# Kernel tuning notes

Measured on AMD Instinct MI355X. Metric: run time of the kernel, lower is better.

Reference implementation:

```python
import jax, jax.numpy as jnp
import numpy as np
from math import factorial

LMAX = 4
N_COEFF = (LMAX + 1) ** 2      # 25 real spherical-harmonic coefficients
N_RADII = 300                  # distance_bins
N_NODES = 512
FEAT = 128
RES_BETA, RES_ALPHA = 180, 360
DIST_STEP = 0.05


def _sh_basis(lmax, y, alpha):
    """Real spherical harmonics evaluated on a (beta, alpha) product grid.
    y = cos(beta) quadrature nodes. Returns [res_beta, res_alpha, (lmax+1)^2]."""
    B, A = len(y), len(alpha)
    P = np.zeros((lmax + 1, lmax + 1, B))
    P[0, 0] = 1.0
    s = np.sqrt(np.clip(1.0 - y * y, 0.0, None))
    for m in range(1, lmax + 1):
        P[m, m] = -(2 * m - 1) * s * P[m - 1, m - 1]
    for m in range(lmax):
        P[m + 1, m] = (2 * m + 1) * y * P[m, m]
    for m in range(lmax + 1):
        for l in range(m + 2, lmax + 1):
            P[l, m] = ((2 * l - 1) * y * P[l - 1, m] - (l + m - 1) * P[l - 2, m]) / (l - m)
    cols = []
    for l in range(lmax + 1):
        for m in range(-l, l + 1):
            am = abs(m)
            Nlm = np.sqrt((2 * l + 1) / (4 * np.pi) * factorial(l - am) / factorial(l + am))
            if m == 0:
                col = Nlm * P[l, 0][:, None] * np.ones((1, A))
            elif m > 0:
                col = np.sqrt(2.0) * Nlm * P[l, m][:, None] * np.cos(m * alpha)[None, :]
            else:
                col = np.sqrt(2.0) * Nlm * P[l, am][:, None] * np.sin(am * alpha)[None, :]
            cols.append(col)
    return np.stack(cols, axis=-1).astype(np.float32)


def setup_inputs() -> dict:
    key = jax.random.key(0)
    ks = jax.random.split(key, 14)

    def lin(k, a, b):
        return jax.random.normal(k, (a, b), jnp.float32) / np.float32(np.sqrt(a))

    x = jax.random.normal(ks[0], (N_NODES, FEAT), jnp.float32)
    fd = [FEAT, 128, 128, 64, 16, 2]
    td = [FEAT, 128, 128, 128, 128, 128, 6]
    fW = [lin(ks[1 + i], fd[i], fd[i + 1]) for i in range(5)]
    tW = [lin(ks[6 + i], td[i], td[i + 1]) for i in range(6)]
    pos_w = lin(ks[12], 2 * FEAT, N_RADII * N_COEFF)
    type_emb = jax.random.normal(ks[13], (5, FEAT), jnp.float32)

    y_np, w_np = np.polynomial.legendre.leggauss(RES_BETA)
    alpha_np = np.linspace(0.0, 2.0 * np.pi, RES_ALPHA, endpoint=False)
    basis = jnp.asarray(_sh_basis(LMAX, y_np, alpha_np))          # [B, A, C]
    qw = jnp.asarray(w_np / 2.0, jnp.float32)                     # gausslegendre / 2
    y_grid = jnp.asarray(y_np, jnp.float32)
    alpha_grid = jnp.asarray(alpha_np, jnp.float32)

    return {
        "x": x,
        "focus_w1": fW[0], "focus_w2": fW[1], "focus_w3": fW[2], "focus_w4": fW[3], "focus_w5": fW[4],
        "type_w1": tW[0], "type_w2": tW[1], "type_w3": tW[2], "type_w4": tW[3], "type_w5": tW[4], "type_w6": tW[5],
        "pos_w": pos_w, "type_emb": type_emb,
        "basis": basis, "qw": qw, "y_grid": y_grid, "alpha_grid": alpha_grid,
        "res_beta": RES_BETA, "res_alpha": RES_ALPHA,
    }


def reference(x, focus_w1, focus_w2, focus_w3, focus_w4, focus_w5,
              type_w1, type_w2, type_w3, type_w4, type_w5, type_w6,
              pos_w, type_emb, basis, qw, y_grid, alpha_grid,
              res_beta, res_alpha):
    n_nodes = x.shape[0]

    # --- focus MLP (relu), per-node logits; STOP logit 0 appended ---
    h = x
    for W in (focus_w1, focus_w2, focus_w3, focus_w4):
        h = jax.nn.relu(h @ W)
    focus_scores = (h @ focus_w5)[:, 0]                             # [n_nodes]
    focus_probs = jax.nn.softmax(jnp.concatenate([focus_scores, jnp.zeros((1,), x.dtype)]))
    focus = jnp.minimum(jnp.argmax(focus_probs), n_nodes - 1)

    # --- type MLP (softplus) on the focus node's features ---
    feat_f = x[focus]                                               # [128]
    th = feat_f
    for W in (type_w1, type_w2, type_w3, type_w4, type_w5):
        th = jax.nn.softplus(th @ W)
    type_dist = jax.nn.softmax(th @ type_w6)                        # [6]
    type_idx = jnp.minimum(jnp.argmax(type_dist), 4)

    # --- position head: SH coefficients per radial shell ---
    pos_in = jnp.concatenate([feat_f, type_emb[type_idx]])          # [256]
    coeffs = (pos_in @ pos_w).reshape(N_RADII, N_COEFF)             # [R, C]

    # to_s2grid: log-density on the sphere for every radial shell
    f = jnp.einsum('rc,bac->rba', coeffs, basis)                    # [R, B, A]
    log_meas = jnp.log(qw)[:, None] + jnp.log(2.0 * jnp.pi / res_alpha)  # [B, 1]

    # radial distribution: integral of exp(f) over the sphere, per shell
    log_radial = jax.nn.logsumexp(f + log_meas[None], axis=(1, 2))  # [R]
    radial_probs = jax.nn.softmax(log_radial)

    key = jax.random.key(42)
    k_r, k_a = jax.random.split(key)
    r_idx = jax.random.categorical(k_r, log_radial)

    # angular distribution at the sampled radius, normalized on S2
    fr = f[r_idx]                                                   # [B, A]
    logZr = jax.nn.logsumexp(fr + log_meas)
    angular_dist = jnp.exp(fr - logZr)                              # [B, A]

    joint_log = (fr + log_meas - logZr).reshape(-1)
    idx = jax.random.categorical(k_a, joint_log)
    y_i = idx // res_alpha
    a_i = idx % res_alpha

    radius_pred = (r_idx.astype(jnp.float32) + 1.0) * DIST_STEP
    return (type_dist, radial_probs, angular_dist, radius_pred, y_grid[y_i], alpha_grid[a_i])
```

## Files before the change

kernel.cpp:

```cpp
#include <hip/hip_runtime.h>
#include <math.h>
#include <stdint.h>

#define NNODES 512
#define FEAT   128
#define NR     300
#define NC     25
#define NB     180
#define NA     360
#define RSPLIT 4
#define BCHUNK (NB / RSPLIT)
#define O_TYPE   0
#define O_RAD    6
#define O_ANG    306
#define O_RADIUS 65106
#define O_Y      65107
#define O_ALPHA  65108

#define WS_KEYS   0
#define WS_FOCUS  4
#define WS_TYPEI  5
#define WS_RIDX   6
#define WS_INVZ   7
#define WS_DEAD   8
#define WS_SCORES 320
#define WS_POSIN  832
#define WS_PV     1280
#define WS_PI     1472
#define WS_Q      1664
#define WS_HR     6176
#define WS_COEF   8352
#define WS_LRP    15872

#define G1_MLP   64
#define G1_PREP  18
#define G1_PFT   21
#define G1_PFP   240
#define G1_TOTAL (G1_MLP + G1_PREP + G1_PFT + G1_PFP)

__constant__ int c_m_of_c[25] = {0,-1,0,1,-2,-1,0,1,2,-3,-2,-1,0,1,2,3,-4,-3,-2,-1,0,1,2,3,4};
__constant__ int c_h_cnt[9] = {5,4,3,2,1,4,3,2,1};
__constant__ int c_h_idx[9][5] = {
  {0,2,6,12,20},
  {3,7,13,21,0},
  {8,14,22,0,0},
  {15,23,0,0,0},
  {24,0,0,0,0},
  {1,5,11,19,0},
  {4,10,18,0,0},
  {9,17,0,0,0},
  {16,0,0,0,0}};

__device__ __forceinline__ void tf2x32(uint32_t k0, uint32_t k1, uint32_t x0, uint32_t x1,
                                       uint32_t& o0, uint32_t& o1) {
  uint32_t ks2 = k0 ^ k1 ^ 0x1BD11BDAu;
#define TF_RND(r) { x0 += x1; x1 = (x1 << r) | (x1 >> (32 - r)); x1 ^= x0; }
  x0 += k0; x1 += k1;
  TF_RND(13) TF_RND(15) TF_RND(26) TF_RND(6)
  x0 += k1; x1 += ks2 + 1u;
  TF_RND(17) TF_RND(29) TF_RND(16) TF_RND(24)
  x0 += ks2; x1 += k0 + 2u;
  TF_RND(13) TF_RND(15) TF_RND(26) TF_RND(6)
  x0 += k0; x1 += k1 + 3u;
  TF_RND(17) TF_RND(29) TF_RND(16) TF_RND(24)
  x0 += k1; x1 += ks2 + 4u;
  TF_RND(13) TF_RND(15) TF_RND(26) TF_RND(6)
  x0 += ks2; x1 += k0 + 5u;
#undef TF_RND
  o0 = x0; o1 = x1;
}

__device__ __forceinline__ float gumbel32(uint32_t k0, uint32_t k1, uint32_t lo) {
  uint32_t o0, o1; tf2x32(k0, k1, 0u, lo, o0, o1);
  uint32_t bits = o0 ^ o1;
  float u = __uint_as_float((bits >> 9) | 0x3f800000u) - 1.0f;
  u = fmaxf(u, 1.1754944e-38f);
  return -logf(-logf(u));
}

__global__ __launch_bounds__(256) void k_front(const float* __restrict__ x,
    const float* __restrict__ w1, const float* __restrict__ w2, const float* __restrict__ w3,
    const float* __restrict__ w4, const float* __restrict__ w5,
    const float* __restrict__ basis, const float* __restrict__ alpha_grid,
    const float* __restrict__ tw1, const float* __restrict__ tw2, const float* __restrict__ tw3,
    const float* __restrict__ tw4, const float* __restrict__ tw5, const float* __restrict__ tw6,
    const float* __restrict__ pos_w,
    float* __restrict__ wsf) {
  __shared__ float A[8][128];
  __shared__ float B[8][128];
  int bx = blockIdx.x, t = threadIdx.x;

  if (bx < G1_MLP) {
    int base = bx * 8;
    for (int i = t; i < 8 * 128; i += 256) A[i >> 7][i & 127] = x[(base + (i >> 7)) * FEAT + (i & 127)];
    __syncthreads();
    int j = t & 127, h = t >> 7;
    {
      float a0 = 0, a1 = 0, a2 = 0, a3 = 0;
#pragma unroll 8
      for (int k = 0; k < 128; k++) {
        float wv = w1[k * 128 + j];
        a0 += A[h * 4 + 0][k] * wv; a1 += A[h * 4 + 1][k] * wv;
        a2 += A[h * 4 + 2][k] * wv; a3 += A[h * 4 + 3][k] * wv;
      }
      __syncthreads();
      B[h * 4 + 0][j] = fmaxf(a0, 0.f); B[h * 4 + 1][j] = fmaxf(a1, 0.f);
      B[h * 4 + 2][j] = fmaxf(a2, 0.f); B[h * 4 + 3][j] = fmaxf(a3, 0.f);
      __syncthreads();
    }
    {
      float a0 = 0, a1 = 0, a2 = 0, a3 = 0;
#pragma unroll 8
      for (int k = 0; k < 128; k++) {
        float wv = w2[k * 128 + j];
        a0 += B[h * 4 + 0][k] * wv; a1 += B[h * 4 + 1][k] * wv;
        a2 += B[h * 4 + 2][k] * wv; a3 += B[h * 4 + 3][k] * wv;
      }
      __syncthreads();
      A[h * 4 + 0][j] = fmaxf(a0, 0.f); A[h * 4 + 1][j] = fmaxf(a1, 0.f);
      A[h * 4 + 2][j] = fmaxf(a2, 0.f); A[h * 4 + 3][j] = fmaxf(a3, 0.f);
      __syncthreads();
    }
    {
      int j3 = t & 63, g = t >> 6;
      float a0 = 0, a1 = 0;
#pragma unroll 8
      for (int k = 0; k < 128; k++) {
        float wv = w3[k * 64 + j3];
        a0 += A[g * 2 + 0][k] * wv; a1 += A[g * 2 + 1][k] * wv;
      }
      __syncthreads();
      B[g * 2 + 0][j3] = fmaxf(a0, 0.f); B[g * 2 + 1][j3] = fmaxf(a1, 0.f);
      __syncthreads();
    }
    {
      int j4 = t & 15, g4 = t >> 4;
      if (g4 < 8) {
        float a0 = 0;
#pragma unroll
        for (int k = 0; k < 64; k++) a0 += B[g4][k] * w4[k * 16 + j4];
        A[g4][j4] = fmaxf(a0, 0.f);
      }
      __syncthreads();
    }
    if (t < 8) {
      float a0 = 0;
#pragma unroll
      for (int k = 0; k < 16; k++) a0 += A[t][k] * w5[k * 2 + 0];
      wsf[WS_SCORES + base + t] = a0;
    }
  } else if (bx < G1_MLP + G1_PREP) {
    int p = (bx - G1_MLP) * 256 + t;
    if (bx == G1_MLP && t == 0) {
      uint32_t* wu = (uint32_t*)wsf;
      uint32_t o0, o1;
      tf2x32(0u, 42u, 0u, 0u, o0, o1); wu[WS_KEYS + 0] = o0; wu[WS_KEYS + 1] = o1;
      tf2x32(0u, 42u, 0u, 1u, o0, o1); wu[WS_KEYS + 2] = o0; wu[WS_KEYS + 3] = o1;
    }
    if (p < NB * NC) {
      int b = p / NC, c = p % NC;
      int m = c_m_of_c[c];
      float q;
      if (m >= 0) {
        q = basis[(b * NA + 0) * NC + c];
      } else {
        float a10 = alpha_grid[10];
        q = basis[(b * NA + 10) * NC + c] / sinf((float)(-m) * a10);
      }
      wsf[WS_Q + p] = q;
    }
  } else if (bx < G1_MLP + G1_PREP + G1_PFT) {
    const float4* mats[5] = {(const float4*)tw1, (const float4*)tw2, (const float4*)tw3,
                             (const float4*)tw4, (const float4*)tw5};
    int lid = (bx - (G1_MLP + G1_PREP)) * 256 + t;
    float acc = 0.f;
    for (int vi = lid; vi < 20672; vi += G1_PFT * 256) {
      int mi = vi >> 12;
      float4 v;
      if (mi < 5) v = mats[mi][vi & 4095];
      else        v = ((const float4*)tw6)[vi - 20480];
      acc += v.x + v.y + v.z + v.w;
    }
    if (acc == -1.2345678e30f) wsf[WS_DEAD] = acc;
  } else {
    int lid = (bx - (G1_MLP + G1_PREP + G1_PFT)) * 256 + t;
    const float4* p4 = (const float4*)pos_w;
    float acc = 0.f;
    for (int i = lid; i < NR * NC * 256 / 4; i += G1_PFP * 256) {
      float4 v = p4[i];
      acc += v.x + v.y + v.z + v.w;
    }
    if (acc == -1.2345678e30f) wsf[WS_DEAD] = acc;
  }
}

__global__ __launch_bounds__(1024) void k_type(const float* __restrict__ x,
    const float* __restrict__ w1, const float* __restrict__ w2, const float* __restrict__ w3,
    const float* __restrict__ w4, const float* __restrict__ w5, const float* __restrict__ w6,
    const float* __restrict__ type_emb, float* __restrict__ out, float* __restrict__ wsf) {
  __shared__ float src[128];
  __shared__ float partial[8][128];
  __shared__ float wrv[16]; __shared__ int wri[16];
  __shared__ float lg[6];
  __shared__ int f_sh, ti_sh;
  int t = threadIdx.x;
  int lane = t & 63, wid = t >> 6;
  float bv = -INFINITY; int bi = 1 << 30;
  if (t < NNODES + 1) { bv = (t < NNODES) ? wsf[WS_SCORES + t] : 0.f; bi = t; }
  for (int off = 32; off; off >>= 1) {
    float v2 = __shfl_down(bv, off); int i2 = __shfl_down(bi, off);
    if (v2 > bv || (v2 == bv && i2 < bi)) { bv = v2; bi = i2; }
  }
  if (lane == 0) { wrv[wid] = bv; wri[wid] = bi; }
  __syncthreads();
  if (t == 0) {
    float v0 = wrv[0]; int i0 = wri[0];
    for (int w = 1; w < 16; w++)
      if (wrv[w] > v0 || (wrv[w] == v0 && wri[w] < i0)) { v0 = wrv[w]; i0 = wri[w]; }
    int focus = (i0 < NNODES - 1) ? i0 : (NNODES - 1);
    ((int*)wsf)[WS_FOCUS] = focus;
    f_sh = focus;
  }
  __syncthreads();
  int focus = f_sh;
  if (t < 128) { float xv = x[focus * FEAT + t]; src[t] = xv; wsf[WS_POSIN + t] = xv; }
  __syncthreads();
  const float* Ws[5] = {w1, w2, w3, w4, w5};
#pragma unroll
  for (int L = 0; L < 5; L++) {
    const float* W = Ws[L];
    int j = t & 127, kc = t >> 7;
    float acc = 0.f;
#pragma unroll
    for (int k = 0; k < 16; k++) acc += src[kc * 16 + k] * W[(kc * 16 + k) * 128 + j];
    partial[kc][j] = acc;
    __syncthreads();
    if (t < 128) {
      float s = 0.f;
#pragma unroll
      for (int q = 0; q < 8; q++) s += partial[q][t];
      src[t] = fmaxf(s, 0.f) + log1pf(expf(-fabsf(s)));
    }
    __syncthreads();
  }
  float prod = 0.f;
  if (t < 768) { int o = t >> 7, j = t & 127; prod = src[j] * w6[j * 6 + o]; }
  for (int off = 32; off; off >>= 1) prod += __shfl_down(prod, off);
  if (t < 768 && lane == 0) wrv[wid] = prod;
  __syncthreads();
  if (t == 0) {
    for (int o = 0; o < 6; o++) lg[o] = wrv[2 * o] + wrv[2 * o + 1];
    float M = lg[0]; int am = 0;
    for (int i = 1; i < 6; i++) if (lg[i] > M) { M = lg[i]; am = i; }
    float e[6], S = 0.f;
    for (int i = 0; i < 6; i++) { e[i] = expf(lg[i] - M); S += e[i]; }
    for (int i = 0; i < 6; i++) out[O_TYPE + i] = e[i] / S;
    int ti = (am < 4) ? am : 4;
    ((int*)wsf)[WS_TYPEI] = ti;
    ti_sh = ti;
  }
  __syncthreads();
  if (t < 128) wsf[WS_POSIN + 128 + t] = type_emb[ti_sh * FEAT + t];
}

__global__ __launch_bounds__(256) void k_coeffs(const float* __restrict__ pos_w,
                                                float* __restrict__ wsf) {
  __shared__ float pin[256];
  __shared__ float partial[4][64];
  int t = threadIdx.x;
  pin[t] = wsf[WS_POSIN + t];
  __syncthreads();
  int oL = t & 63, kc = t >> 6;
  int o = blockIdx.x * 64 + oL;
  float acc = 0.f;
  if (o < NR * NC) {
#pragma unroll 16
    for (int k = 0; k < 64; k++) acc += pin[kc * 64 + k] * pos_w[(kc * 64 + k) * (NR * NC) + o];
  }
  partial[kc][oL] = acc;
  __syncthreads();
  if (kc == 0 && o < NR * NC)
    wsf[WS_COEF + o] = partial[0][oL] + partial[1][oL] + partial[2][oL] + partial[3][oL];
}

__global__ __launch_bounds__(384) void k_radial_lse(const float* __restrict__ qw,
    const float* __restrict__ alpha_grid, float* __restrict__ wsf) {
  __shared__ float4 Hs4[BCHUNK * 3];
  __shared__ float cs[NC];
  __shared__ float wred[6];
  int bx = blockIdx.x;
  int r = bx >> 2, s = bx & 3;
  int b0 = s * BCHUNK;
  int t = threadIdx.x;
  float* Hs = (float*)Hs4;
  if (t < NC) cs[t] = wsf[WS_COEF + r * NC + t];
  __syncthreads();
  const float LOGM = -4.0482054576f;
  for (int p = t; p < BCHUNK * 9; p += 384) {
    int b = p / 9, jj = p % 9;
    int bg = b0 + b;
    int n = c_h_cnt[jj];
    float acc = 0.f;
    for (int q = 0; q < n; q++) { int c = c_h_idx[jj][q]; acc += cs[c] * wsf[WS_Q + bg * NC + c]; }
    if (jj == 0) acc += logf(qw[bg]) + LOGM;
    Hs[b * 12 + jj] = acc;
  }
  __syncthreads();
  float c1 = 0, c2 = 0, c3 = 0, c4 = 0, s1 = 0, s2 = 0, s3 = 0, s4 = 0;
  bool act = t < NA;
  if (act) {
    float al = alpha_grid[t];
    sincosf(al, &s1, &c1);
    sincosf(2.f * al, &s2, &c2);
    sincosf(3.f * al, &s3, &c3);
    sincosf(4.f * al, &s4, &c4);
  }
  float acc = 0.f;
#pragma unroll 5
  for (int b = 0; b < BCHUNK; b++) {
    float4 h0 = Hs4[b * 3 + 0], h1 = Hs4[b * 3 + 1], h2 = Hs4[b * 3 + 2];
    float f = h0.x + h0.y * c1 + h0.z * c2 + h0.w * c3 + h1.x * c4
            + h1.y * s1 + h1.z * s2 + h1.w * s3 + h2.x * s4;
    acc += act ? __expf(f) : 0.f;
  }
  for (int off = 32; off; off >>= 1) acc += __shfl_down(acc, off);
  int wid = t >> 6, lane = t & 63;
  if (lane == 0) wred[wid] = acc;
  __syncthreads();
  if (t == 0) {
    float ss = 0.f;
    for (int w = 0; w < 6; w++) ss += wred[w];
    wsf[WS_LRP + bx] = ss;
  }
}

__global__ __launch_bounds__(384) void k_radial_sample(float* __restrict__ out,
                                                       float* __restrict__ wsf) {
  __shared__ float wred[6]; __shared__ int wri[6];
  __shared__ float fss[NR];
  __shared__ float S_sh; __shared__ int r_sh;
  int t = threadIdx.x, lane = t & 63, wid = t >> 6;
  const uint32_t* wu = (const uint32_t*)wsf;
  uint32_t kr0 = wu[WS_KEYS + 0], kr1 = wu[WS_KEYS + 1];
  float sv = 0.f, lr = -INFINITY;
  if (t < NR) {
    sv = wsf[WS_LRP + 4 * t] + wsf[WS_LRP + 4 * t + 1]
       + wsf[WS_LRP + 4 * t + 2] + wsf[WS_LRP + 4 * t + 3];
    fss[t] = sv;
    lr = logf(sv);
  }
  float ss = sv;
  for (int off = 32; off; off >>= 1) ss += __shfl_down(ss, off);
  if (lane == 0) wred[wid] = ss;
  __syncthreads();
  if (t == 0) {
    float S = 0.f;
    for (int w = 0; w < 6; w++) S += wred[w];
    S_sh = S;
  }
  __syncthreads();
  if (t < NR) out[O_RAD + t] = sv / S_sh;
  float v = (t < NR) ? lr + gumbel32(kr0, kr1, (uint32_t)t) : -INFINITY;
  int bi = (t < NR) ? t : (1 << 30);
  for (int off = 32; off; off >>= 1) {
    float v2 = __shfl_down(v, off); int i2 = __shfl_down(bi, off);
    if (v2 > v || (v2 == v && i2 < bi)) { v = v2; bi = i2; }
  }
  __syncthreads();
  if (lane == 0) { wred[wid] = v; wri[wid] = bi; }
  __syncthreads();
  if (t == 0) {
    float v0 = wred[0]; int i0 = wri[0];
    for (int w = 1; w < 6; w++)
      if (wred[w] > v0 || (wred[w] == v0 && wri[w] < i0)) { v0 = wred[w]; i0 = wri[w]; }
    r_sh = i0;
    ((int*)wsf)[WS_RIDX] = i0;
    out[O_RADIUS] = (float)(i0 + 1) * 0.05f;
    wsf[WS_INVZ] = 1.0f / fss[i0];
  }
  __syncthreads();
  int r = r_sh;
  for (int p = t; p < NB * 9; p += 384) {
    int b = p / 9, jj = p % 9, n = c_h_cnt[jj];
    float acc = 0.f;
    for (int q = 0; q < n; q++) {
      int c = c_h_idx[jj][q];
      acc += wsf[WS_COEF + r * NC + c] * wsf[WS_Q + b * NC + c];
    }
    wsf[WS_HR + b * 12 + jj] = acc;
  }
}

__global__ __launch_bounds__(384) void k_ang_partial(const float* __restrict__ qw,
    const float* __restrict__ alpha_grid, float* __restrict__ out, float* __restrict__ wsf) {
  __shared__ float wrv[6]; __shared__ int wri[6];
  int b = blockIdx.x, t = threadIdx.x;
  int lane = t & 63, wid = t >> 6;
  const uint32_t* wu = (const uint32_t*)wsf;
  uint32_t ka0 = wu[WS_KEYS + 2], ka1 = wu[WS_KEYS + 3];
  const float4* hr4 = (const float4*)(wsf + WS_HR + b * 12);
  float4 h0 = hr4[0], h1 = hr4[1], h2 = hr4[2];
  const float MEAS = 0.01745329252f;
  float elm = qw[b] * MEAS;
  float lm = logf(elm);
  float invZ = wsf[WS_INVZ];
  float v = -INFINITY; int idx = (t < NA) ? b * NA + t : (1 << 30);
  if (t < NA) {
    float al = alpha_grid[t];
    float s1, c1, s2, c2, s3, c3, s4, c4;
    sincosf(al, &s1, &c1); sincosf(2.f * al, &s2, &c2);
    sincosf(3.f * al, &s3, &c3); sincosf(4.f * al, &s4, &c4);
    float f = h0.x + h0.y * c1 + h0.z * c2 + h0.w * c3 + h1.x * c4
            + h1.y * s1 + h1.z * s2 + h1.w * s3 + h2.x * s4;
    out[O_ANG + idx] = __expf(f) * invZ;
    v = f + lm + gumbel32(ka0, ka1, (uint32_t)idx);
  }
  for (int off = 32; off; off >>= 1) {
    float v2 = __shfl_down(v, off); int i2 = __shfl_down(idx, off);
    if (v2 > v || (v2 == v && i2 < idx)) { v = v2; idx = i2; }
  }
  if (lane == 0) { wrv[wid] = v; wri[wid] = idx; }
  __syncthreads();
  if (t == 0) {
    float v0 = wrv[0]; int i0 = wri[0];
    for (int w = 1; w < 6; w++)
      if (wrv[w] > v0 || (wrv[w] == v0 && wri[w] < i0)) { v0 = wrv[w]; i0 = wri[w]; }
    wsf[WS_PV + b] = v0;
    ((int*)wsf)[WS_PI + b] = i0;
  }
}

__global__ __launch_bounds__(256) void k_ang_final(const float* __restrict__ y_grid,
    const float* __restrict__ alpha_grid, float* __restrict__ out, float* __restrict__ wsf) {
  __shared__ float wr[4]; __shared__ int wi[4];
  int t = threadIdx.x, lane = t & 63, wid = t >> 6;
  float v = (t < NB) ? wsf[WS_PV + t] : -INFINITY;
  int i = (t < NB) ? ((const int*)wsf)[WS_PI + t] : (1 << 30);
  for (int off = 32; off; off >>= 1) {
    float v2 = __shfl_down(v, off); int i2 = __shfl_down(i, off);
    if (v2 > v || (v2 == v && i2 < i)) { v = v2; i = i2; }
  }
  if (lane == 0) { wr[wid] = v; wi[wid] = i; }
  __syncthreads();
  if (t == 0) {
    float v0 = wr[0]; int i0 = wi[0];
    for (int w = 1; w < 4; w++)
      if (wr[w] > v0 || (wr[w] == v0 && wi[w] < i0)) { v0 = wr[w]; i0 = wi[w]; }
    int yi = i0 / NA, ai = i0 % NA;
    out[O_Y] = y_grid[yi];
    out[O_ALPHA] = alpha_grid[ai];
  }
}

extern "C" void kernel_launch(void* const* d_in, const int* in_sizes, int n_in,
                              void* d_out, int out_size, void* d_ws, size_t ws_size,
                              hipStream_t stream) {
  const float* x          = (const float*)d_in[0];
  const float* fw1        = (const float*)d_in[1];
  const float* fw2        = (const float*)d_in[2];
  const float* fw3        = (const float*)d_in[3];
  const float* fw4        = (const float*)d_in[4];
  const float* fw5        = (const float*)d_in[5];
  const float* tw1        = (const float*)d_in[6];
  const float* tw2        = (const float*)d_in[7];
  const float* tw3        = (const float*)d_in[8];
  const float* tw4        = (const float*)d_in[9];
  const float* tw5        = (const float*)d_in[10];
  const float* tw6        = (const float*)d_in[11];
  const float* pos_w      = (const float*)d_in[12];
  const float* type_emb   = (const float*)d_in[13];
  const float* basis      = (const float*)d_in[14];
  const float* qw         = (const float*)d_in[15];
  const float* y_grid     = (const float*)d_in[16];
  const float* alpha_grid = (const float*)d_in[17];
  (void)in_sizes; (void)n_in; (void)out_size; (void)ws_size;
  float* out = (float*)d_out;
  float* wsf = (float*)d_ws;

  k_front<<<G1_TOTAL, 256, 0, stream>>>(x, fw1, fw2, fw3, fw4, fw5, basis, alpha_grid,
                                        tw1, tw2, tw3, tw4, tw5, tw6, pos_w, wsf);
  k_type<<<1, 1024, 0, stream>>>(x, tw1, tw2, tw3, tw4, tw5, tw6, type_emb, out, wsf);
  k_coeffs<<<(NR * NC + 63) / 64, 256, 0, stream>>>(pos_w, wsf);
  k_radial_lse<<<NR * RSPLIT, 384, 0, stream>>>(qw, alpha_grid, wsf);
  k_radial_sample<<<1, 384, 0, stream>>>(out, wsf);
  k_ang_partial<<<NB, 384, 0, stream>>>(qw, alpha_grid, out, wsf);
  k_ang_final<<<1, 256, 0, stream>>>(y_grid, alpha_grid, out, wsf);
}
```

Measured before the change: 63.79 us.

## Fuse seven-kernel pipeline into one cooperative kernel with grid syncs

Replaces the chain of seven dependent kernel launches with a single cooperative kernel of 256 blocks, using grid.sync() between the MLP/prep, type head, coefficient GEMV, radial LSE, radial sampling, angular partial and final argmax stages. The aim is to remove per-launch overhead and inter-kernel gaps, which are large relative to this small workload. In exchange, the radial LSE stage now loops over 1200 tasks on 256 blocks, the MLP stage uses smaller per-block tiles, and serial single-block phases leave most of the grid idle at each barrier. The old launch sequence remains as a fallback if the cooperative launch fails.

```diff
diff --git a/kernel.cpp b/kernel.cpp
--- a/kernel.cpp
+++ b/kernel.cpp
@@ -1,6 +1,9 @@
 #include <hip/hip_runtime.h>
+#include <hip/hip_cooperative_groups.h>
 #include <math.h>
 #include <stdint.h>
+
+namespace cg = cooperative_groups;
 
 #define NNODES 512
 #define FEAT   128
@@ -31,6 +34,9 @@
 #define WS_HR     6176
 #define WS_COEF   8352
 #define WS_LRP    15872
+
+#define CG_BLOCKS 256
+#define CG_THREADS 384
 
 #define G1_MLP   64
 #define G1_PREP  18
@@ -78,6 +84,375 @@
   return -logf(-logf(u));
 }
 
+__device__ __forceinline__ float softplusf(float s) {
+  return fmaxf(s, 0.f) + log1pf(expf(-fabsf(s)));
+}
+
+__global__ __launch_bounds__(CG_THREADS) void k_all(
+    const float* __restrict__ x,
+    const float* __restrict__ fw1, const float* __restrict__ fw2, const float* __restrict__ fw3,
+    const float* __restrict__ fw4, const float* __restrict__ fw5,
+    const float* __restrict__ tw1, const float* __restrict__ tw2, const float* __restrict__ tw3,
+    const float* __restrict__ tw4, const float* __restrict__ tw5, const float* __restrict__ tw6,
+    const float* __restrict__ pos_w, const float* __restrict__ type_emb,
+    const float* __restrict__ basis, const float* __restrict__ qw,
+    const float* __restrict__ y_grid, const float* __restrict__ alpha_grid,
+    float* __restrict__ out, float* __restrict__ wsf) {
+  __shared__ float S0[4][128];
+  __shared__ float S1[4][128];
+  __shared__ float4 HS[BCHUNK * 3];
+  __shared__ float cs[32];
+  __shared__ float wred[8]; __shared__ int wri[8];
+  __shared__ float lg[8];
+  __shared__ float fsh[2];
+  __shared__ int ish[2];
+  cg::grid_group grid = cg::this_grid();
+  int bx = blockIdx.x, t = threadIdx.x;
+  int lane = t & 63, wid = t >> 6;
+
+  if (bx < 128) {
+    int base = bx * 4;
+    for (int i = t; i < 512; i += CG_THREADS)
+      S0[i >> 7][i & 127] = x[(base + (i >> 7)) * FEAT + (i & 127)];
+    __syncthreads();
+    int j = t & 127, h = t >> 7;
+    float a0 = 0.f, a1 = 0.f;
+    if (h < 2) {
+#pragma unroll 8
+      for (int k = 0; k < 128; k++) {
+        float wv = fw1[k * 128 + j];
+        a0 += S0[h * 2 + 0][k] * wv; a1 += S0[h * 2 + 1][k] * wv;
+      }
+    }
+    __syncthreads();
+    if (h < 2) { S1[h * 2 + 0][j] = fmaxf(a0, 0.f); S1[h * 2 + 1][j] = fmaxf(a1, 0.f); }
+    __syncthreads();
+    a0 = a1 = 0.f;
+    if (h < 2) {
+#pragma unroll 8
+      for (int k = 0; k < 128; k++) {
+        float wv = fw2[k * 128 + j];
+        a0 += S1[h * 2 + 0][k] * wv; a1 += S1[h * 2 + 1][k] * wv;
+      }
+    }
+    __syncthreads();
+    if (h < 2) { S0[h * 2 + 0][j] = fmaxf(a0, 0.f); S0[h * 2 + 1][j] = fmaxf(a1, 0.f); }
+    __syncthreads();
+    {
+      int j3 = t & 63, g = t >> 6;
+      float a = 0.f;
+      if (g < 4) {
+#pragma unroll 8
+        for (int k = 0; k < 128; k++) a += S0[g][k] * fw3[k * 64 + j3];
+      }
+      __syncthreads();
+      if (g < 4) S1[g][j3] = fmaxf(a, 0.f);
+      __syncthreads();
+    }
+    {
+      int j4 = t & 15, g4 = t >> 4;
+      if (g4 < 4) {
+        float a = 0.f;
+#pragma unroll
+        for (int k = 0; k < 64; k++) a += S1[g4][k] * fw4[k * 16 + j4];
+        S0[g4][j4] = fmaxf(a, 0.f);
+      }
+      __syncthreads();
+    }
+    if (t < 4) {
+      float a = 0.f;
+#pragma unroll
+      for (int k = 0; k < 16; k++) a += S0[t][k] * fw5[k * 2 + 0];
+      wsf[WS_SCORES + base + t] = a;
+    }
+  } else if (bx < 146) {
+    if (bx == 128 && t == 383) {
+      uint32_t* wu = (uint32_t*)wsf;
+      uint32_t o0, o1;
+      tf2x32(0u, 42u, 0u, 0u, o0, o1); wu[WS_KEYS + 0] = o0; wu[WS_KEYS + 1] = o1;
+      tf2x32(0u, 42u, 0u, 1u, o0, o1); wu[WS_KEYS + 2] = o0; wu[WS_KEYS + 3] = o1;
+    }
+    if (t < 256) {
+      int p = (bx - 128) * 256 + t;
+      if (p < NB * NC) {
+        int b = p / NC, c = p % NC;
+        int m = c_m_of_c[c];
+        float q;
+        if (m >= 0) {
+          q = basis[(b * NA + 0) * NC + c];
+        } else {
+          float a10 = alpha_grid[10];
+          q = basis[(b * NA + 10) * NC + c] / sinf((float)(-m) * a10);
+        }
+        wsf[WS_Q + p] = q;
+      }
+    } else {
+      const float4* mats[5] = {(const float4*)tw1, (const float4*)tw2, (const float4*)tw3,
+                               (const float4*)tw4, (const float4*)tw5};
+      int lid = (bx - 128) * 128 + (t - 256);
+      float acc = 0.f;
+      for (int vi = lid; vi < 20672; vi += 18 * 128) {
+        int mi = vi >> 12;
+        float4 v;
+        if (mi < 5) v = mats[mi][vi & 4095];
+        else        v = ((const float4*)tw6)[vi - 20480];
+        acc += v.x + v.y + v.z + v.w;
+      }
+      if (acc == -1.2345678e30f) wsf[WS_DEAD] = acc;
+    }
+  } else {
+    int lid = (bx - 146) * CG_THREADS + t;
+    const float4* p4 = (const float4*)pos_w;
+    float acc = 0.f;
+    for (int i = lid; i < NR * NC * 256 / 4; i += 110 * CG_THREADS) {
+      float4 v = p4[i];
+      acc += v.x + v.y + v.z + v.w;
+    }
+    if (acc == -1.2345678e30f) wsf[WS_DEAD] = acc;
+  }
+  grid.sync();
+
+  if (bx == 0) {
+    float bv = -INFINITY; int bi = 1 << 30;
+    for (int i = t; i < NNODES + 1; i += CG_THREADS) {
+      float v = (i < NNODES) ? wsf[WS_SCORES + i] : 0.f;
+      if (v > bv || (v == bv && i < bi)) { bv = v; bi = i; }
+    }
+    for (int off = 32; off; off >>= 1) {
+      float v2 = __shfl_down(bv, off); int i2 = __shfl_down(bi, off);
+      if (v2 > bv || (v2 == bv && i2 < bi)) { bv = v2; bi = i2; }
+    }
+    if (lane == 0) { wred[wid] = bv; wri[wid] = bi; }
+    __syncthreads();
+    if (t == 0) {
+      float v0 = wred[0]; int i0 = wri[0];
+      for (int w = 1; w < 6; w++)
+        if (wred[w] > v0 || (wred[w] == v0 && wri[w] < i0)) { v0 = wred[w]; i0 = wri[w]; }
+      int focus = (i0 < NNODES - 1) ? i0 : (NNODES - 1);
+      ((int*)wsf)[WS_FOCUS] = focus;
+      ish[0] = focus;
+    }
+    __syncthreads();
+    int focus = ish[0];
+    float* src = &S0[0][0];
+    if (t < 128) { float xv = x[focus * FEAT + t]; src[t] = xv; wsf[WS_POSIN + t] = xv; }
+    __syncthreads();
+    const float* Ws[5] = {tw1, tw2, tw3, tw4, tw5};
+    int kc = t >> 7, j = t & 127;
+#pragma unroll
+    for (int L = 0; L < 5; L++) {
+      const float* W = Ws[L];
+      float acc = 0.f;
+      if (t < 256) {
+#pragma unroll 8
+        for (int k = 0; k < 64; k++) { int kk = kc * 64 + k; acc += src[kk] * W[kk * 128 + j]; }
+        S1[kc][j] = acc;
+      }
+      __syncthreads();
+      if (t < 128) src[t] = softplusf(S1[0][t] + S1[1][t]);
+      __syncthreads();
+    }
+    {
+      int o = t >> 6, l = t & 63;
+      float pr = src[l] * tw6[l * 6 + o] + src[l + 64] * tw6[(l + 64) * 6 + o];
+      for (int off = 32; off; off >>= 1) pr += __shfl_down(pr, off);
+      if (lane == 0) lg[o] = pr;
+    }
+    __syncthreads();
+    if (t == 0) {
+      float M = lg[0]; int am = 0;
+      for (int i = 1; i < 6; i++) if (lg[i] > M) { M = lg[i]; am = i; }
+      float e[6], S = 0.f;
+      for (int i = 0; i < 6; i++) { e[i] = expf(lg[i] - M); S += e[i]; }
+      for (int i = 0; i < 6; i++) out[O_TYPE + i] = e[i] / S;
+      int ti = (am < 4) ? am : 4;
+      ((int*)wsf)[WS_TYPEI] = ti;
+      ish[1] = ti;
+    }
+    __syncthreads();
+    if (t < 128) wsf[WS_POSIN + 128 + t] = type_emb[ish[1] * FEAT + t];
+  }
+  grid.sync();
+
+  if (bx < 118) {
+    float* pin = &S0[0][0];
+    float* part = &S1[0][0];
+    if (t < 256) pin[t] = wsf[WS_POSIN + t];
+    __syncthreads();
+    int oL = t & 63, kc = (t >> 6) & 3;
+    int o = bx * 64 + oL;
+    if (t < 256) {
+      float acc = 0.f;
+      if (o < NR * NC) {
+#pragma unroll 16
+        for (int k = 0; k < 64; k++) { int kk = kc * 64 + k; acc += pin[kk] * pos_w[kk * (NR * NC) + o]; }
+      }
+      part[kc * 64 + oL] = acc;
+    }
+    __syncthreads();
+    if (t < 64 && o < NR * NC)
+      wsf[WS_COEF + o] = part[oL] + part[64 + oL] + part[128 + oL] + part[192 + oL];
+  }
+  grid.sync();
+
+  {
+    float c1 = 0, c2 = 0, c3 = 0, c4 = 0, s1 = 0, s2 = 0, s3 = 0, s4 = 0;
+    bool act = t < NA;
+    if (act) {
+      float al = alpha_grid[t];
+      sincosf(al, &s1, &c1);
+      sincosf(2.f * al, &s2, &c2);
+      sincosf(3.f * al, &s3, &c3);
+      sincosf(4.f * al, &s4, &c4);
+    }
+    const float LOGM = -4.0482054576f;
+    float* Hs = (float*)HS;
+    for (int task = bx; task < NR * RSPLIT; task += CG_BLOCKS) {
+      int r = task >> 2, sb = task & 3, b0 = sb * BCHUNK;
+      __syncthreads();
+      if (t < NC) cs[t] = wsf[WS_COEF + r * NC + t];
+      __syncthreads();
+      for (int p = t; p < BCHUNK * 9; p += CG_THREADS) {
+        int b = p / 9, jj = p % 9;
+        int bg = b0 + b;
+        int n = c_h_cnt[jj];
+        float acc = 0.f;
+        for (int q = 0; q < n; q++) { int c = c_h_idx[jj][q]; acc += cs[c] * wsf[WS_Q + bg * NC + c]; }
+        if (jj == 0) acc += logf(qw[bg]) + LOGM;
+        Hs[b * 12 + jj] = acc;
+      }
+      __syncthreads();
+      float acc = 0.f;
+#pragma unroll 5
+      for (int b = 0; b < BCHUNK; b++) {
+        float4 h0 = HS[b * 3 + 0], h1 = HS[b * 3 + 1], h2 = HS[b * 3 + 2];
+        float f = h0.x + h0.y * c1 + h0.z * c2 + h0.w * c3 + h1.x * c4
+                + h1.y * s1 + h1.z * s2 + h1.w * s3 + h2.x * s4;
+        acc += act ? __expf(f) : 0.f;
+      }
+      for (int off = 32; off; off >>= 1) acc += __shfl_down(acc, off);
+      if (lane == 0) wred[wid] = acc;
+      __syncthreads();
+      if (t == 0) {
+        float ss = 0.f;
+        for (int w = 0; w < 6; w++) ss += wred[w];
+        wsf[WS_LRP + task] = ss;
+      }
+    }
+  }
+  grid.sync();
+
+  if (bx == 0) {
+    const uint32_t* wu = (const uint32_t*)wsf;
+    uint32_t kr0 = wu[WS_KEYS + 0], kr1 = wu[WS_KEYS + 1];
+    float* fss = &S0[0][0];
+    float sv = 0.f, lr = -INFINITY;
+    if (t < NR) {
+      sv = wsf[WS_LRP + 4 * t] + wsf[WS_LRP + 4 * t + 1]
+         + wsf[WS_LRP + 4 * t + 2] + wsf[WS_LRP + 4 * t + 3];
+      fss[t] = sv;
+      lr = logf(sv);
+    }
+    float ss = sv;
+    for (int off = 32; off; off >>= 1) ss += __shfl_down(ss, off);
+    if (lane == 0) wred[wid] = ss;
+    __syncthreads();
+    if (t == 0) {
+      float S = 0.f;
+      for (int w = 0; w < 6; w++) S += wred[w];
+      fsh[0] = S;
+    }
+    __syncthreads();
+    if (t < NR) out[O_RAD + t] = sv / fsh[0];
+    float v = (t < NR) ? lr + gumbel32(kr0, kr1, (uint32_t)t) : -INFINITY;
+    int bi = (t < NR) ? t : (1 << 30);
+    for (int off = 32; off; off >>= 1) {
+      float v2 = __shfl_down(v, off); int i2 = __shfl_down(bi, off);
+      if (v2 > v || (v2 == v && i2 < bi)) { v = v2; bi = i2; }
+    }
+    __syncthreads();
+    if (lane == 0) { wred[wid] = v; wri[wid] = bi; }
+    __syncthreads();
+    if (t == 0) {
+      float v0 = wred[0]; int i0 = wri[0];
+      for (int w = 1; w < 6; w++)
+        if (wred[w] > v0 || (wred[w] == v0 && wri[w] < i0)) { v0 = wred[w]; i0 = wri[w]; }
+      ish[0] = i0;
+      ((int*)wsf)[WS_RIDX] = i0;
+      out[O_RADIUS] = (float)(i0 + 1) * 0.05f;
+      wsf[WS_INVZ] = 1.0f / fss[i0];
+    }
+    __syncthreads();
+    int r = ish[0];
+    for (int p = t; p < NB * 9; p += CG_THREADS) {
+      int b = p / 9, jj = p % 9, n = c_h_cnt[jj];
+      float acc = 0.f;
+      for (int q = 0; q < n; q++) {
+        int c = c_h_idx[jj][q];
+        acc += wsf[WS_COEF + r * NC + c] * wsf[WS_Q + b * NC + c];
+      }
+      wsf[WS_HR + b * 12 + jj] = acc;
+    }
+  }
+  grid.sync();
+
+  if (bx < NB) {
+    int b = bx;
+    const uint32_t* wu = (const uint32_t*)wsf;
+    uint32_t ka0 = wu[WS_KEYS + 2], ka1 = wu[WS_KEYS + 3];
+    const float4* hr4 = (const float4*)(wsf + WS_HR + b * 12);
+    float4 h0 = hr4[0], h1 = hr4[1], h2 = hr4[2];
+    const float MEAS = 0.01745329252f;
+    float elm = qw[b] * MEAS;
+    float lm = logf(elm);
+    float invZ = wsf[WS_INVZ];
+    float v = -INFINITY; int idx = (t < NA) ? b * NA + t : (1 << 30);
+    if (t < NA) {
+      float al = alpha_grid[t];
+      float s1, c1, s2, c2, s3, c3, s4, c4;
+      sincosf(al, &s1, &c1); sincosf(2.f * al, &s2, &c2);
+      sincosf(3.f * al, &s3, &c3); sincosf(4.f * al, &s4, &c4);
+      float f = h0.x + h0.y * c1 + h0.z * c2 + h0.w * c3 + h1.x * c4
+              + h1.y * s1 + h1.z * s2 + h1.w * s3 + h2.x * s4;
+      out[O_ANG + idx] = __expf(f) * invZ;
+      v = f + lm + gumbel32(ka0, ka1, (uint32_t)idx);
+    }
+    for (int off = 32; off; off >>= 1) {
+      float v2 = __shfl_down(v, off); int i2 = __shfl_down(idx, off);
+      if (v2 > v || (v2 == v && i2 < idx)) { v = v2; idx = i2; }
+    }
+    if (lane == 0) { wred[wid] = v; wri[wid] = idx; }
+    __syncthreads();
+    if (t == 0) {
+      float v0 = wred[0]; int i0 = wri[0];
+      for (int w = 1; w < 6; w++)
+        if (wred[w] > v0 || (wred[w] == v0 && wri[w] < i0)) { v0 = wred[w]; i0 = wri[w]; }
+      wsf[WS_PV + b] = v0;
+      ((int*)wsf)[WS_PI + b] = i0;
+    }
+  }
+  grid.sync();
+
+  if (bx == 0) {
+    float v = (t < NB) ? wsf[WS_PV + t] : -INFINITY;
+    int i = (t < NB) ? ((const int*)wsf)[WS_PI + t] : (1 << 30);
+    for (int off = 32; off; off >>= 1) {
+      float v2 = __shfl_down(v, off); int i2 = __shfl_down(i, off);
+      if (v2 > v || (v2 == v && i2 < i)) { v = v2; i = i2; }
+    }
+    if (lane == 0) { wred[wid] = v; wri[wid] = i; }
+    __syncthreads();
+    if (t == 0) {
+      float v0 = wred[0]; int i0 = wri[0];
+      for (int w = 1; w < 6; w++)
+        if (wred[w] > v0 || (wred[w] == v0 && wri[w] < i0)) { v0 = wred[w]; i0 = wri[w]; }
+      int yi = i0 / NA, ai = i0 % NA;
+      out[O_Y] = y_grid[yi];
+      out[O_ALPHA] = alpha_grid[ai];
+    }
+  }
+}
+
 __global__ __launch_bounds__(256) void k_front(const float* __restrict__ x,
     const float* __restrict__ w1, const float* __restrict__ w2, const float* __restrict__ w3,
     const float* __restrict__ w4, const float* __restrict__ w5,
@@ -89,7 +464,6 @@
   __shared__ float A[8][128];
   __shared__ float B[8][128];
   int bx = blockIdx.x, t = threadIdx.x;
-
   if (bx < G1_MLP) {
     int base = bx * 8;
     for (int i = t; i < 8 * 128; i += 256) A[i >> 7][i & 127] = x[(base + (i >> 7)) * FEAT + (i & 127)];
@@ -147,7 +521,7 @@
       float a0 = 0;
 #pragma unroll
       for (int k = 0; k < 16; k++) a0 += A[t][k] * w5[k * 2 + 0];
-      wsf[WS_SCORES + base + t] = a0;
+      wsf[WS_SCORES + bx * 8 + t] = a0;
     }
   } else if (bx < G1_MLP + G1_PREP) {
     int p = (bx - G1_MLP) * 256 + t;
@@ -161,9 +535,8 @@
       int b = p / NC, c = p % NC;
       int m = c_m_of_c[c];
       float q;
-      if (m >= 0) {
-        q = basis[(b * NA + 0) * NC + c];
-      } else {
+      if (m >= 0) q = basis[(b * NA + 0) * NC + c];
+      else {
         float a10 = alpha_grid[10];
         q = basis[(b * NA + 10) * NC + c] / sinf((float)(-m) * a10);
       }
@@ -200,7 +573,7 @@
     const float* __restrict__ type_emb, float* __restrict__ out, float* __restrict__ wsf) {
   __shared__ float src[128];
   __shared__ float partial[8][128];
-  __shared__ float wrv[16]; __shared__ int wri[16];
+  __shared__ float wrv[16]; __shared__ int wri2[16];
   __shared__ float lg[6];
   __shared__ int f_sh, ti_sh;
   int t = threadIdx.x;
@@ -211,12 +584,12 @@
     float v2 = __shfl_down(bv, off); int i2 = __shfl_down(bi, off);
     if (v2 > bv || (v2 == bv && i2 < bi)) { bv = v2; bi = i2; }
   }
-  if (lane == 0) { wrv[wid] = bv; wri[wid] = bi; }
+  if (lane == 0) { wrv[wid] = bv; wri2[wid] = bi; }
   __syncthreads();
   if (t == 0) {
-    float v0 = wrv[0]; int i0 = wri[0];
+    float v0 = wrv[0]; int i0 = wri2[0];
     for (int w = 1; w < 16; w++)
-      if (wrv[w] > v0 || (wrv[w] == v0 && wri[w] < i0)) { v0 = wrv[w]; i0 = wri[w]; }
+      if (wrv[w] > v0 || (wrv[w] == v0 && wri2[w] < i0)) { v0 = wrv[w]; i0 = wri2[w]; }
     int focus = (i0 < NNODES - 1) ? i0 : (NNODES - 1);
     ((int*)wsf)[WS_FOCUS] = focus;
     f_sh = focus;
@@ -239,7 +612,7 @@
       float s = 0.f;
 #pragma unroll
       for (int q = 0; q < 8; q++) s += partial[q][t];
-      src[t] = fmaxf(s, 0.f) + log1pf(expf(-fabsf(s)));
+      src[t] = softplusf(s);
     }
     __syncthreads();
   }
@@ -336,7 +709,7 @@
 
 __global__ __launch_bounds__(384) void k_radial_sample(float* __restrict__ out,
                                                        float* __restrict__ wsf) {
-  __shared__ float wred[6]; __shared__ int wri[6];
+  __shared__ float wred[6]; __shared__ int wri2[6];
   __shared__ float fss[NR];
   __shared__ float S_sh; __shared__ int r_sh;
   int t = threadIdx.x, lane = t & 63, wid = t >> 6;
@@ -367,12 +740,12 @@
     if (v2 > v || (v2 == v && i2 < bi)) { v = v2; bi = i2; }
   }
   __syncthreads();
-  if (lane == 0) { wred[wid] = v; wri[wid] = bi; }
+  if (lane == 0) { wred[wid] = v; wri2[wid] = bi; }
   __syncthreads();
   if (t == 0) {
-    float v0 = wred[0]; int i0 = wri[0];
+    float v0 = wred[0]; int i0 = wri2[0];
     for (int w = 1; w < 6; w++)
-      if (wred[w] > v0 || (wred[w] == v0 && wri[w] < i0)) { v0 = wred[w]; i0 = wri[w]; }
+      if (wred[w] > v0 || (wred[w] == v0 && wri2[w] < i0)) { v0 = wred[w]; i0 = wri2[w]; }
     r_sh = i0;
     ((int*)wsf)[WS_RIDX] = i0;
     out[O_RADIUS] = (float)(i0 + 1) * 0.05f;
@@ -393,7 +766,7 @@
 
 __global__ __launch_bounds__(384) void k_ang_partial(const float* __restrict__ qw,
     const float* __restrict__ alpha_grid, float* __restrict__ out, float* __restrict__ wsf) {
-  __shared__ float wrv[6]; __shared__ int wri[6];
+  __shared__ float wrv[6]; __shared__ int wri2[6];
   int b = blockIdx.x, t = threadIdx.x;
   int lane = t & 63, wid = t >> 6;
   const uint32_t* wu = (const uint32_t*)wsf;
@@ -419,12 +792,12 @@
     float v2 = __shfl_down(v, off); int i2 = __shfl_down(idx, off);
     if (v2 > v || (v2 == v && i2 < idx)) { v = v2; idx = i2; }
   }
-  if (lane == 0) { wrv[wid] = v; wri[wid] = idx; }
+  if (lane == 0) { wrv[wid] = v; wri2[wid] = idx; }
   __syncthreads();
   if (t == 0) {
-    float v0 = wrv[0]; int i0 = wri[0];
+    float v0 = wrv[0]; int i0 = wri2[0];
     for (int w = 1; w < 6; w++)
-      if (wrv[w] > v0 || (wrv[w] == v0 && wri[w] < i0)) { v0 = wrv[w]; i0 = wri[w]; }
+      if (wrv[w] > v0 || (wrv[w] == v0 && wri2[w] < i0)) { v0 = wrv[w]; i0 = wri2[w]; }
     wsf[WS_PV + b] = v0;
     ((int*)wsf)[WS_PI + b] = i0;
   }
@@ -477,12 +850,20 @@
   float* out = (float*)d_out;
   float* wsf = (float*)d_ws;
 
-  k_front<<<G1_TOTAL, 256, 0, stream>>>(x, fw1, fw2, fw3, fw4, fw5, basis, alpha_grid,
-                                        tw1, tw2, tw3, tw4, tw5, tw6, pos_w, wsf);
-  k_type<<<1, 1024, 0, stream>>>(x, tw1, tw2, tw3, tw4, tw5, tw6, type_emb, out, wsf);
-  k_coeffs<<<(NR * NC + 63) / 64, 256, 0, stream>>>(pos_w, wsf);
-  k_radial_lse<<<NR * RSPLIT, 384, 0, stream>>>(qw, alpha_grid, wsf);
-  k_radial_sample<<<1, 384, 0, stream>>>(out, wsf);
-  k_ang_partial<<<NB, 384, 0, stream>>>(qw, alpha_grid, out, wsf);
-  k_ang_final<<<1, 256, 0, stream>>>(y_grid, alpha_grid, out, wsf);
-}
+  void* kargs[] = {(void*)&x, (void*)&fw1, (void*)&fw2, (void*)&fw3, (void*)&fw4, (void*)&fw5,
+                   (void*)&tw1, (void*)&tw2, (void*)&tw3, (void*)&tw4, (void*)&tw5, (void*)&tw6,
+                   (void*)&pos_w, (void*)&type_emb, (void*)&basis, (void*)&qw,
+                   (void*)&y_grid, (void*)&alpha_grid, (void*)&out, (void*)&wsf};
+  hipError_t err = hipLaunchCooperativeKernel((const void*)k_all, dim3(CG_BLOCKS), dim3(CG_THREADS),
+                                              kargs, 0, stream);
+  if (err != hipSuccess) {
+    k_front<<<G1_TOTAL, 256, 0, stream>>>(x, fw1, fw2, fw3, fw4, fw5, basis, alpha_grid,
+                                          tw1, tw2, tw3, tw4, tw5, tw6, pos_w, wsf);
+    k_type<<<1, 1024, 0, stream>>>(x, tw1, tw2, tw3, tw4, tw5, tw6, type_emb, out, wsf);
+    k_coeffs<<<(NR * NC + 63) / 64, 256, 0, stream>>>(pos_w, wsf);
+    k_radial_lse<<<NR * RSPLIT, 384, 0, stream>>>(qw, alpha_grid, wsf);
+    k_radial_sample<<<1, 384, 0, stream>>>(out, wsf);
+    k_ang_partial<<<NB, 384, 0, stream>>>(qw, alpha_grid, out, wsf);
+    k_ang_final<<<1, 256, 0, stream>>>(y_grid, alpha_grid, out, wsf);
+  }
+}
```

Result: slower. 239.4 us (+275.3%).

## Fuse coefficient GEMV into radial and angular kernels, drop k_coeffs launch

Applied to the files above, without the earlier changes.

Removes the separate k_coeffs kernel and instead has each radial-LSE block compute the 25 coefficients for its own radius from pos_w and the pos-input vector. The per-row harmonic reduction is also moved out of k_radial_sample: each angular block recomputes the sampled radius's coefficients and its row's 9 harmonic sums. This removes one launch, the coefficient round trip through global memory, and the serial tail loop in the single-block sample kernel. In exchange every block redundantly reads 256 strided pos_w columns, four times per radius in the radial kernel and 180 times in the angular kernel.

```diff
diff --git a/kernel.cpp b/kernel.cpp
--- a/kernel.cpp
+++ b/kernel.cpp
@@ -28,9 +28,7 @@
 #define WS_PV     1280
 #define WS_PI     1472
 #define WS_Q      1664
-#define WS_HR     6176
-#define WS_COEF   8352
-#define WS_LRP    15872
+#define WS_LRP    6176
 
 #define G1_MLP   64
 #define G1_PREP  18
@@ -78,6 +76,10 @@
   return -logf(-logf(u));
 }
 
+__device__ __forceinline__ float softplusf(float s) {
+  return fmaxf(s, 0.f) + log1pf(expf(-fabsf(s)));
+}
+
 __global__ __launch_bounds__(256) void k_front(const float* __restrict__ x,
     const float* __restrict__ w1, const float* __restrict__ w2, const float* __restrict__ w3,
     const float* __restrict__ w4, const float* __restrict__ w5,
@@ -239,7 +241,7 @@
       float s = 0.f;
 #pragma unroll
       for (int q = 0; q < 8; q++) s += partial[q][t];
-      src[t] = fmaxf(s, 0.f) + log1pf(expf(-fabsf(s)));
+      src[t] = softplusf(s);
     }
     __syncthreads();
   }
@@ -263,38 +265,42 @@
   if (t < 128) wsf[WS_POSIN + 128 + t] = type_emb[ti_sh * FEAT + t];
 }
 
-__global__ __launch_bounds__(256) void k_coeffs(const float* __restrict__ pos_w,
-                                                float* __restrict__ wsf) {
+__device__ __forceinline__ void coeffs_for_r(const float* __restrict__ pos_w,
+                                             const float* __restrict__ pin,
+                                             float (*part)[32], float* cs, int r, int t) {
+  int kk = t >> 5, c = t & 31;
+  float acc = 0.f;
+  if (c < NC) {
+    const float* col = pos_w + r * NC + c;
+    for (int k = kk; k < 256; k += 12) acc += pin[k] * col[k * (NR * NC)];
+  }
+  part[kk][c] = acc;
+  __syncthreads();
+  if (t < NC) {
+    float a = 0.f;
+#pragma unroll
+    for (int kk2 = 0; kk2 < 12; kk2++) a += part[kk2][t];
+    cs[t] = a;
+  }
+  __syncthreads();
+}
+
+__global__ __launch_bounds__(384) void k_radial_lse(const float* __restrict__ pos_w,
+    const float* __restrict__ qw, const float* __restrict__ alpha_grid,
+    float* __restrict__ wsf) {
   __shared__ float pin[256];
-  __shared__ float partial[4][64];
-  int t = threadIdx.x;
-  pin[t] = wsf[WS_POSIN + t];
-  __syncthreads();
-  int oL = t & 63, kc = t >> 6;
-  int o = blockIdx.x * 64 + oL;
-  float acc = 0.f;
-  if (o < NR * NC) {
-#pragma unroll 16
-    for (int k = 0; k < 64; k++) acc += pin[kc * 64 + k] * pos_w[(kc * 64 + k) * (NR * NC) + o];
-  }
-  partial[kc][oL] = acc;
-  __syncthreads();
-  if (kc == 0 && o < NR * NC)
-    wsf[WS_COEF + o] = partial[0][oL] + partial[1][oL] + partial[2][oL] + partial[3][oL];
-}
-
-__global__ __launch_bounds__(384) void k_radial_lse(const float* __restrict__ qw,
-    const float* __restrict__ alpha_grid, float* __restrict__ wsf) {
+  __shared__ float part[12][32];
+  __shared__ float cs[NC];
   __shared__ float4 Hs4[BCHUNK * 3];
-  __shared__ float cs[NC];
   __shared__ float wred[6];
   int bx = blockIdx.x;
   int r = bx >> 2, s = bx & 3;
   int b0 = s * BCHUNK;
   int t = threadIdx.x;
   float* Hs = (float*)Hs4;
-  if (t < NC) cs[t] = wsf[WS_COEF + r * NC + t];
-  __syncthreads();
+  if (t < 256) pin[t] = wsf[WS_POSIN + t];
+  __syncthreads();
+  coeffs_for_r(pos_w, pin, part, cs, r, t);
   const float LOGM = -4.0482054576f;
   for (int p = t; p < BCHUNK * 9; p += 384) {
     int b = p / 9, jj = p % 9;
@@ -338,7 +344,7 @@
                                                        float* __restrict__ wsf) {
   __shared__ float wred[6]; __shared__ int wri[6];
   __shared__ float fss[NR];
-  __shared__ float S_sh; __shared__ int r_sh;
+  __shared__ float S_sh;
   int t = threadIdx.x, lane = t & 63, wid = t >> 6;
   const uint32_t* wu = (const uint32_t*)wsf;
   uint32_t kr0 = wu[WS_KEYS + 0], kr1 = wu[WS_KEYS + 1];
@@ -373,33 +379,35 @@
     float v0 = wred[0]; int i0 = wri[0];
     for (int w = 1; w < 6; w++)
       if (wred[w] > v0 || (wred[w] == v0 && wri[w] < i0)) { v0 = wred[w]; i0 = wri[w]; }
-    r_sh = i0;
     ((int*)wsf)[WS_RIDX] = i0;
     out[O_RADIUS] = (float)(i0 + 1) * 0.05f;
     wsf[WS_INVZ] = 1.0f / fss[i0];
   }
-  __syncthreads();
-  int r = r_sh;
-  for (int p = t; p < NB * 9; p += 384) {
-    int b = p / 9, jj = p % 9, n = c_h_cnt[jj];
-    float acc = 0.f;
-    for (int q = 0; q < n; q++) {
-      int c = c_h_idx[jj][q];
-      acc += wsf[WS_COEF + r * NC + c] * wsf[WS_Q + b * NC + c];
-    }
-    wsf[WS_HR + b * 12 + jj] = acc;
-  }
-}
-
-__global__ __launch_bounds__(384) void k_ang_partial(const float* __restrict__ qw,
-    const float* __restrict__ alpha_grid, float* __restrict__ out, float* __restrict__ wsf) {
+}
+
+__global__ __launch_bounds__(384) void k_ang_partial(const float* __restrict__ pos_w,
+    const float* __restrict__ qw, const float* __restrict__ alpha_grid,
+    float* __restrict__ out, float* __restrict__ wsf) {
+  __shared__ float pin[256];
+  __shared__ float part[12][32];
+  __shared__ float cs[NC];
+  __shared__ float hsh[12];
   __shared__ float wrv[6]; __shared__ int wri[6];
   int b = blockIdx.x, t = threadIdx.x;
   int lane = t & 63, wid = t >> 6;
   const uint32_t* wu = (const uint32_t*)wsf;
   uint32_t ka0 = wu[WS_KEYS + 2], ka1 = wu[WS_KEYS + 3];
-  const float4* hr4 = (const float4*)(wsf + WS_HR + b * 12);
-  float4 h0 = hr4[0], h1 = hr4[1], h2 = hr4[2];
+  int r = ((const int*)wsf)[WS_RIDX];
+  if (t < 256) pin[t] = wsf[WS_POSIN + t];
+  __syncthreads();
+  coeffs_for_r(pos_w, pin, part, cs, r, t);
+  if (t < 9) {
+    int n = c_h_cnt[t];
+    float acc = 0.f;
+    for (int q = 0; q < n; q++) { int c = c_h_idx[t][q]; acc += cs[c] * wsf[WS_Q + b * NC + c]; }
+    hsh[t] = acc;
+  }
+  __syncthreads();
   const float MEAS = 0.01745329252f;
   float elm = qw[b] * MEAS;
   float lm = logf(elm);
@@ -410,8 +418,8 @@
     float s1, c1, s2, c2, s3, c3, s4, c4;
     sincosf(al, &s1, &c1); sincosf(2.f * al, &s2, &c2);
     sincosf(3.f * al, &s3, &c3); sincosf(4.f * al, &s4, &c4);
-    float f = h0.x + h0.y * c1 + h0.z * c2 + h0.w * c3 + h1.x * c4
-            + h1.y * s1 + h1.z * s2 + h1.w * s3 + h2.x * s4;
+    float f = hsh[0] + hsh[1] * c1 + hsh[2] * c2 + hsh[3] * c3 + hsh[4] * c4
+            + hsh[5] * s1 + hsh[6] * s2 + hsh[7] * s3 + hsh[8] * s4;
     out[O_ANG + idx] = __expf(f) * invZ;
     v = f + lm + gumbel32(ka0, ka1, (uint32_t)idx);
   }
@@ -480,9 +488,8 @@
   k_front<<<G1_TOTAL, 256, 0, stream>>>(x, fw1, fw2, fw3, fw4, fw5, basis, alpha_grid,
                                         tw1, tw2, tw3, tw4, tw5, tw6, pos_w, wsf);
   k_type<<<1, 1024, 0, stream>>>(x, tw1, tw2, tw3, tw4, tw5, tw6, type_emb, out, wsf);
-  k_coeffs<<<(NR * NC + 63) / 64, 256, 0, stream>>>(pos_w, wsf);
-  k_radial_lse<<<NR * RSPLIT, 384, 0, stream>>>(qw, alpha_grid, wsf);
+  k_radial_lse<<<NR * RSPLIT, 384, 0, stream>>>(pos_w, qw, alpha_grid, wsf);
   k_radial_sample<<<1, 384, 0, stream>>>(out, wsf);
-  k_ang_partial<<<NB, 384, 0, stream>>>(qw, alpha_grid, out, wsf);
+  k_ang_partial<<<NB, 384, 0, stream>>>(pos_w, qw, alpha_grid, out, wsf);
   k_ang_final<<<1, 256, 0, stream>>>(y_grid, alpha_grid, out, wsf);
 }
```

Measured after the change: 76.55 us. +20.0%, slower.
